# Optimization experiments

Measured on AMD Instinct MI355X. Metric: run time of the kernel, lower is better.

## Reference

```python
import jax, jax.numpy as jnp
import numpy as np
import math

FACTOR = 5  # Informer 'factor' hyperparameter


def setup_inputs() -> dict:
    key = jax.random.key(0)
    B, L, H, D = 2, 2048, 16, 128
    k1, k2, k3, k4 = jax.random.split(key, 4)
    queries = jax.random.normal(k1, (B, L, H, D), jnp.float32)
    keys = jax.random.normal(k2, (B, L, H, D), jnp.float32)
    values = jax.random.normal(k3, (B, L, H, D), jnp.float32)
    sample_k = max(1, min(FACTOR * math.ceil(math.log(L)), L))  # u in the paper
    index_sample = jax.random.randint(k4, (L, sample_k), 0, L, dtype=jnp.int32)
    return {"queries": queries, "keys": keys, "values": values,
            "index_sample": index_sample}


def reference(queries, keys, values, index_sample):
    # queries/keys/values: [B, L, H, D] -> [B, H, L, D]
    Q = jnp.swapaxes(queries, 1, 2)
    K = jnp.swapaxes(keys, 1, 2)
    V = jnp.swapaxes(values, 1, 2)
    B, H, L_Q, D = Q.shape
    L_K = K.shape[2]
    # U_part = factor*ceil(ln L_K), clipped to L_K then to L_Q (n_top in _prob_QK)
    n_top = max(1, min(FACTOR * math.ceil(math.log(L_K)), L_K, L_Q))

    # --- _prob_QK: sampled scores ---
    # K_sample: [B, H, L_Q, sample_k, D] (same materialization as torch K_expand gather)
    K_sample = K[:, :, index_sample, :]
    Q_K_sample = jnp.einsum('bhqd,bhqsd->bhqs', Q, K_sample)
    # sparsity measure M: max - mean(over full L_K, per original torch code)
    M = Q_K_sample.max(axis=-1) - Q_K_sample.sum(axis=-1) / L_K  # [B,H,L_Q]
    _, M_top = jax.lax.top_k(M, n_top)  # [B,H,n_top]

    # gather top queries and compute their full attention rows
    Q_reduce = jnp.take_along_axis(Q, M_top[..., None], axis=2)  # [B,H,u,D]
    scores = jnp.einsum('bhud,bhkd->bhuk', Q_reduce, K)  # [B,H,u,L_K]
    scale = 1.0 / math.sqrt(D)
    scores = scores * scale

    # --- initial context (mask_flag=False): mean of V over keys ---
    context = jnp.broadcast_to(V.mean(axis=2, keepdims=True), (B, H, L_Q, D))

    # --- update context at top-query positions ---
    attn = jax.nn.softmax(scores, axis=-1)
    upd = jnp.einsum('bhuk,bhkd->bhud', attn, V)  # [B,H,u,D]
    bi = jnp.arange(B)[:, None, None]
    hi = jnp.arange(H)[None, :, None]
    context = context.at[bi, hi, M_top].set(upd)

    return jnp.swapaxes(context, 1, 2)  # [B, L_Q, H, D]
```

## Files before the change

kernel.cpp:

```cpp
#include <hip/hip_runtime.h>
#include <math.h>

#define B_    2
#define L_    2048
#define H_    16
#define D_    128
#define S_    40
#define NTOP_ 40
#define NCH_  8
#define CHK_  256
#define VCH_  32
#define CAND_ 512

#define SCALE_ 0.08838834764831843f

typedef _Float16 half2_t __attribute__((ext_vector_type(2)));

__device__ __forceinline__ half2_t as_h2(unsigned int u) {
    union { unsigned int u; half2_t h; } x; x.u = u; return x.h;
}
__device__ __forceinline__ unsigned int h2pack(float a, float b) {
    union { half2_t h; unsigned int u; } x;
    x.h[0] = (_Float16)a; x.h[1] = (_Float16)b; return x.u;
}
#if __has_builtin(__builtin_amdgcn_fdot2)
__device__ __forceinline__ float FDOT2(half2_t a, half2_t b, float c) {
    return __builtin_amdgcn_fdot2(a, b, c, false);
}
#else
__device__ __forceinline__ float FDOT2(half2_t a, half2_t b, float c) {
    return c + (float)a[0] * (float)b[0] + (float)a[1] * (float)b[1];
}
#endif

__device__ __forceinline__ unsigned int encf(float f) {
    unsigned int u = __float_as_uint(f);
    return (u & 0x80000000u) ? ~u : (u | 0x80000000u);
}
__device__ __forceinline__ float decf(unsigned int e) {
    unsigned int u = (e & 0x80000000u) ? (e ^ 0x80000000u) : ~e;
    return __uint_as_float(u);
}

__global__ __launch_bounds__(256) void kA_pack_vpart(const float* __restrict__ K,
                                                     const float* __restrict__ V,
                                                     unsigned int* __restrict__ Kf,
                                                     float* __restrict__ vpart,
                                                     int npack) {
    const int bid = blockIdx.x, t = threadIdx.x;
    if (bid < npack) {
        const int bh = bid >> 3, kc = bid & 7;
        const int h = bh & 15, b = bh >> 4;
        const float4* K4 = (const float4*)K;
        uint2* out2 = (uint2*)Kf;
        for (int j = 0; j < 32; ++j) {
            const int g = j * 256 + t;
            const int row = g >> 5, c = g & 31;
            const float4 v = K4[((size_t)(b * L_ + kc * 256 + row) * H_ + h) * 32 + c];
            out2[(size_t)(bh * L_ + kc * 256 + row) * 32 + c] =
                make_uint2(h2pack(v.x, v.y), h2pack(v.z, v.w));
        }
    } else {
        __shared__ float red[256];
        const int vbid = bid - npack;
        const int bh  = vbid >> 5;
        const int lc  = vbid & (VCH_ - 1);
        const int h   = bh & 15, b = bh >> 4;
        const int d   = t & (D_ - 1);
        const int sub = t >> 7;
        float acc = 0.0f;
        const int l0 = lc * (L_ / VCH_);
        for (int l = l0 + sub; l < l0 + L_ / VCH_; l += 2)
            acc += V[((size_t)(b * L_ + l) * H_ + h) * D_ + d];
        red[t] = acc;
        __syncthreads();
        if (t < D_) vpart[(size_t)vbid * D_ + t] = red[t] + red[t + 128];
    }
}

__global__ __launch_bounds__(256) void k1_sample_f16(const float* __restrict__ Q,
                                                     const uint4* __restrict__ KF,
                                                     const int* __restrict__ idx,
                                                     float* __restrict__ M) {
    const int sb   = blockIdx.x;
    const int xcd  = sb & 7;
    const int li   = sb >> 3;
    const int bh   = (xcd << 2) + (li >> 9);
    const int rb   = li & 511;
    const int t    = threadIdx.x;
    const int wave = t >> 6, lane = t & 63;
    const int q    = rb * 4 + wave;
    const int h    = bh & 15, b = bh >> 4;
    const int g    = lane >> 3, sub = lane & 7;

    const float4* Q4 = (const float4*)Q;
    const size_t rowQ = ((size_t)(b * L_ + q) * H_ + h) * 32;
    const int* ip = idx + q * S_;
    int kidx[5];
    #pragma unroll
    for (int s = 0; s < 5; ++s) kidx[s] = ip[s * 8 + g];

    const float4 qa0 = Q4[rowQ + 2 * sub];
    const float4 qa1 = Q4[rowQ + 2 * sub + 1];
    const float4 qb0 = Q4[rowQ + 16 + 2 * sub];
    const float4 qb1 = Q4[rowQ + 16 + 2 * sub + 1];

    uint4 kv[5][2];
    #pragma unroll
    for (int s = 0; s < 5; ++s) {
        const uint4* kr = KF + ((size_t)bh * L_ + kidx[s]) * 16;
        kv[s][0] = kr[sub];
        kv[s][1] = kr[8 + sub];
    }
    __builtin_amdgcn_sched_barrier(0);

    half2_t qh[8];
    qh[0][0] = (_Float16)qa0.x; qh[0][1] = (_Float16)qa0.y;
    qh[1][0] = (_Float16)qa0.z; qh[1][1] = (_Float16)qa0.w;
    qh[2][0] = (_Float16)qa1.x; qh[2][1] = (_Float16)qa1.y;
    qh[3][0] = (_Float16)qa1.z; qh[3][1] = (_Float16)qa1.w;
    qh[4][0] = (_Float16)qb0.x; qh[4][1] = (_Float16)qb0.y;
    qh[5][0] = (_Float16)qb0.z; qh[5][1] = (_Float16)qb0.w;
    qh[6][0] = (_Float16)qb1.x; qh[6][1] = (_Float16)qb1.y;
    qh[7][0] = (_Float16)qb1.z; qh[7][1] = (_Float16)qb1.w;

    float smax = -INFINITY, ssum = 0.0f;
    #pragma unroll
    for (int s = 0; s < 5; ++s) {
        float p = 0.f;
        p = FDOT2(qh[0], as_h2(kv[s][0].x), p);
        p = FDOT2(qh[1], as_h2(kv[s][0].y), p);
        p = FDOT2(qh[2], as_h2(kv[s][0].z), p);
        p = FDOT2(qh[3], as_h2(kv[s][0].w), p);
        p = FDOT2(qh[4], as_h2(kv[s][1].x), p);
        p = FDOT2(qh[5], as_h2(kv[s][1].y), p);
        p = FDOT2(qh[6], as_h2(kv[s][1].z), p);
        p = FDOT2(qh[7], as_h2(kv[s][1].w), p);
        p += __shfl_xor(p, 1);
        p += __shfl_xor(p, 2);
        p += __shfl_xor(p, 4);
        smax = fmaxf(smax, p);
        ssum += p;
    }
    #pragma unroll
    for (int o = 8; o < 64; o <<= 1) {
        smax = fmaxf(smax, __shfl_xor(smax, o));
        ssum += __shfl_xor(ssum, o);
    }
    if (lane == 0) M[(size_t)bh * L_ + q] = smax - ssum * (1.0f / L_);
}

__global__ __launch_bounds__(256) void k1_sample_f32(const float* __restrict__ Q,
                                                     const float* __restrict__ K,
                                                     const int* __restrict__ idx,
                                                     float* __restrict__ M) {
    const int sb   = blockIdx.x;
    const int xcd  = sb & 7;
    const int li   = sb >> 3;
    const int bh   = (xcd << 2) + (li >> 9);
    const int rb   = li & 511;
    const int t    = threadIdx.x;
    const int wave = t >> 6, lane = t & 63;
    const int q    = rb * 4 + wave;
    const int h    = bh & 15, b = bh >> 4;
    const int g    = lane >> 3, sub = lane & 7;

    const float4* Q4 = (const float4*)Q;
    const float4* K4 = (const float4*)K;
    const size_t rowQ = ((size_t)(b * L_ + q) * H_ + h) * 32;
    const size_t kbase = ((size_t)b * L_ * H_ + h) * 32 + sub;
    const int* ip = idx + q * S_;
    int kidx[5];
    #pragma unroll
    for (int s = 0; s < 5; ++s) kidx[s] = ip[s * 8 + g];
    const float4 qv0 = Q4[rowQ + 0 + sub];
    const float4 qv1 = Q4[rowQ + 8 + sub];
    const float4 qv2 = Q4[rowQ + 16 + sub];
    const float4 qv3 = Q4[rowQ + 24 + sub];
    float4 kv[5][4];
    #pragma unroll
    for (int s = 0; s < 5; ++s) {
        const float4* kb = K4 + kbase + (size_t)kidx[s] * (H_ * 32);
        kv[s][0] = kb[0]; kv[s][1] = kb[8]; kv[s][2] = kb[16]; kv[s][3] = kb[24];
    }
    __builtin_amdgcn_sched_barrier(0);
    float smax = -INFINITY, ssum = 0.0f;
    #pragma unroll
    for (int s = 0; s < 5; ++s) {
        float p = qv0.x * kv[s][0].x + qv0.y * kv[s][0].y + qv0.z * kv[s][0].z + qv0.w * kv[s][0].w
                + qv1.x * kv[s][1].x + qv1.y * kv[s][1].y + qv1.z * kv[s][1].z + qv1.w * kv[s][1].w
                + qv2.x * kv[s][2].x + qv2.y * kv[s][2].y + qv2.z * kv[s][2].z + qv2.w * kv[s][2].w
                + qv3.x * kv[s][3].x + qv3.y * kv[s][3].y + qv3.z * kv[s][3].z + qv3.w * kv[s][3].w;
        p += __shfl_xor(p, 1);
        p += __shfl_xor(p, 2);
        p += __shfl_xor(p, 4);
        smax = fmaxf(smax, p);
        ssum += p;
    }
    #pragma unroll
    for (int o = 8; o < 64; o <<= 1) {
        smax = fmaxf(smax, __shfl_xor(smax, o));
        ssum += __shfl_xor(ssum, o);
    }
    if (lane == 0) M[(size_t)bh * L_ + q] = smax - ssum * (1.0f / L_);
}

__global__ __launch_bounds__(1024) void k2_rank_refine(const float* __restrict__ Mws,
                                                       const float* __restrict__ Q,
                                                       const float* __restrict__ K,
                                                       const int* __restrict__ idx,
                                                       const float* __restrict__ vpart,
                                                       float* __restrict__ vmean,
                                                       int* __restrict__ topk,
                                                       float delta) {
    const int bid = blockIdx.x, t = threadIdx.x;
    if (bid == 32) {
        for (int e = t; e < 32 * D_; e += 1024) {
            const int bh = e >> 7, d = e & 127;
            float s = 0.f;
            #pragma unroll
            for (int c = 0; c < VCH_; ++c)
                s += vpart[(size_t)(bh * VCH_ + c) * D_ + d];
            vmean[e] = s * (1.0f / L_);
        }
        return;
    }
    __shared__ unsigned int ue[L_];
    __shared__ int hist[256], sscan[256];
    __shared__ int sh_chosen, sh_need, sh_nc;
    __shared__ int clist[CAND_];
    __shared__ float cMx[CAND_];
    __shared__ unsigned int cmaxe[CAND_];
    __shared__ float csum[CAND_];
    const int bh = bid, h = bh & 15, b = bh >> 4;
    const float* Mrow = Mws + (size_t)bh * L_;
    for (int i = t; i < L_; i += 1024) ue[i] = encf(Mrow[i]);
    if (t == 0) sh_nc = 0;
    __syncthreads();

    unsigned int prefix = 0; int need = NTOP_;
    for (int l = 3; l >= 0; --l) {
        if (t < 256) hist[t] = 0;
        __syncthreads();
        for (int i = t; i < L_; i += 1024) {
            const unsigned int u = ue[i];
            const bool match = (l == 3) || ((u >> (8 * (l + 1))) == prefix);
            if (match) atomicAdd(&hist[(u >> (8 * l)) & 255], 1);
        }
        __syncthreads();
        if (t < 256) sscan[t] = hist[t];
        __syncthreads();
        for (int off = 1; off < 256; off <<= 1) {
            int v = 0;
            if (t < 256 && t + off < 256) v = sscan[t + off];
            __syncthreads();
            if (t < 256) sscan[t] += v;
            __syncthreads();
        }
        if (t < 256) {
            const int above = sscan[t] - hist[t];
            if (above < need && need <= above + hist[t]) { sh_chosen = t; sh_need = need - above; }
        }
        __syncthreads();
        prefix = (prefix << 8) | (unsigned int)sh_chosen;
        need = sh_need;
        __syncthreads();
    }
    const unsigned int ethr = encf(decf(prefix) - delta);
    for (int i = t; i < L_; i += 1024) {
        if (ue[i] >= ethr) {
            const int p = atomicAdd(&sh_nc, 1);
            if (p < CAND_) clist[p] = i;
        }
    }
    __syncthreads();
    const int nc = min(sh_nc, CAND_);
    for (int i = t; i < CAND_; i += 1024) { cmaxe[i] = 0x007FFFFFu; csum[i] = 0.f; }
    __syncthreads();

    const float4* Q4 = (const float4*)Q;
    const float4* K4 = (const float4*)K;
    const int grp = t >> 3, sub = t & 7;
    for (int task = grp; task < nc * S_; task += 128) {
        const int ci = task / S_;
        const int s  = task - ci * S_;
        const int qq = clist[ci];
        const int ki = idx[qq * S_ + s];
        const float4* Kr = K4 + ((size_t)(b * L_ + ki) * H_ + h) * 32;
        const float4* Qr = Q4 + ((size_t)(b * L_ + qq) * H_ + h) * 32;
        float p = 0.f;
        #pragma unroll
        for (int qt2 = 0; qt2 < 4; ++qt2) {
            const float4 kv = Kr[qt2 * 8 + sub];
            const float4 qv = Qr[qt2 * 8 + sub];
            p += qv.x * kv.x + qv.y * kv.y + qv.z * kv.z + qv.w * kv.w;
        }
        p += __shfl_xor(p, 1);
        p += __shfl_xor(p, 2);
        p += __shfl_xor(p, 4);
        if (sub == 0) {
            atomicMax(&cmaxe[ci], encf(p));
            atomicAdd(&csum[ci], p);
        }
    }
    __syncthreads();
    if (t < nc) cMx[t] = decf(cmaxe[t]) - csum[t] * (1.0f / L_);
    __syncthreads();
    if (t < nc) {
        const float mi = cMx[t]; const int qi = clist[t];
        int rk = 0;
        for (int j = 0; j < nc; ++j) {
            const float mj = cMx[j];
            rk += (mj > mi) || (mj == mi && clist[j] < qi);
        }
        if (rk < NTOP_) topk[bh * NTOP_ + rk] = qi;
    }
}

__global__ __launch_bounds__(512) void k3_scorepv_fill(const float* __restrict__ Q,
                                                       const float* __restrict__ K,
                                                       const float* __restrict__ V,
                                                       const int* __restrict__ topk,
                                                       const float* __restrict__ vmean,
                                                       float* __restrict__ pmax,
                                                       float* __restrict__ psum,
                                                       float* __restrict__ pout,
                                                       float* __restrict__ out) {
    __shared__ float Qs[20 * 132];
    __shared__ float S[20 * 260];
    __shared__ float2 Ppv[20][64];
    __shared__ float mrow[20];
    __shared__ int   tq[20];
    const int bid0 = blockIdx.x;
    const int t   = threadIdx.x;

    if (bid0 >= 512) {
        const int fb = bid0 - 512;
        const float4* vm4 = (const float4*)vmean;
        float4* out4 = (float4*)out;
        const size_t base = (size_t)fb * 4096;
        #pragma unroll
        for (int k = 0; k < 8; ++k) {
            const size_t i = base + k * 512 + t;
            const int d4 = (int)(i & 31);
            const int h  = (int)((i >> 5) & 15);
            const int b  = (int)(i >> 20);
            out4[i] = vm4[((b << 4) + h) * 32 + d4];
        }
        return;
    }

    const int xcd = bid0 & 7;
    const int loc = bid0 >> 3;
    const int bh  = (xcd << 2) + (loc >> 4);
    const int sub16 = loc & 15;
    const int kc  = sub16 >> 1;
    const int uh  = sub16 & 1;
    const int h   = bh & 15, b = bh >> 4;
    const int w   = t >> 6, lane = t & 63;

    if (t < 20) tq[t] = topk[bh * NTOP_ + uh * 20 + t];
    __syncthreads();

    {
        const float4* Q4 = (const float4*)Q;
        #pragma unroll
        for (int it = 0; it < 2; ++it) {
            const int i = it * 512 + t;
            if (i < 640) {
                const int u = i >> 5, dc = i & 31;
                *(float4*)&Qs[u * 132 + dc * 4] =
                    Q4[((size_t)(b * L_ + tq[u]) * H_ + h) * 32 + dc];
            }
        }
    }
    __syncthreads();

    {
        const int kq2 = t >> 2, ug = t & 3;
        float acc[2][5];
        #pragma unroll
        for (int j = 0; j < 2; ++j)
            #pragma unroll
            for (int uu = 0; uu < 5; ++uu) acc[j][uu] = 0.f;
        const float4* Kb = (const float4*)K +
            ((size_t)(b * L_ + kc * CHK_ + kq2 * 2) * H_ + h) * 32;
        for (int dc = 0; dc < 32; ++dc) {
            float4 qv[5];
            #pragma unroll
            for (int uu = 0; uu < 5; ++uu)
                qv[uu] = *(const float4*)&Qs[(ug * 5 + uu) * 132 + dc * 4];
            #pragma unroll
            for (int j = 0; j < 2; ++j) {
                const float4 kv = Kb[(size_t)j * (H_ * 32) + dc];
                #pragma unroll
                for (int uu = 0; uu < 5; ++uu)
                    acc[j][uu] += qv[uu].x * kv.x + qv[uu].y * kv.y
                                + qv[uu].z * kv.z + qv[uu].w * kv.w;
            }
        }
        #pragma unroll
        for (int j = 0; j < 2; ++j)
            #pragma unroll
            for (int uu = 0; uu < 5; ++uu)
                S[(ug * 5 + uu) * 260 + kq2 * 2 + j] = acc[j][uu] * SCALE_;
    }
    __syncthreads();

    {
        #pragma unroll
        for (int jj = 0; jj < 3; ++jj) {
            const int u = w + 8 * jj;
            if (u < 20) {
                const float* Sr = S + u * 260;
                float v = fmaxf(fmaxf(Sr[lane], Sr[lane + 64]),
                                fmaxf(Sr[lane + 128], Sr[lane + 192]));
                #pragma unroll
                for (int o = 1; o < 64; o <<= 1) v = fmaxf(v, __shfl_xor(v, o, 64));
                if (lane == 0) mrow[u] = v;
            }
        }
    }
    __syncthreads();

    for (int e = t; e < 20 * 256; e += 512) {
        const int u = e >> 8, k = e & 255;
        S[u * 260 + k] = __expf(S[u * 260 + k] - mrow[u]);
    }
    __syncthreads();

    {
        #pragma unroll
        for (int jj = 0; jj < 3; ++jj) {
            const int u = w + 8 * jj;
            if (u < 20) {
                const float* Sr = S + u * 260;
                float v = Sr[lane] + Sr[lane + 64] + Sr[lane + 128] + Sr[lane + 192];
                #pragma unroll
                for (int o = 1; o < 64; o <<= 1) v += __shfl_xor(v, o, 64);
                if (lane == 0) {
                    psum[(bh * NCH_ + kc) * NTOP_ + uh * 20 + u] = v;
                    pmax[(bh * NCH_ + kc) * NTOP_ + uh * 20 + u] = mrow[u];
                }
            }
        }
    }

    {
        const int kr2 = w & 1, ug2 = w >> 1;
        const int d2 = lane;
        float accA[5], accB[5];
        #pragma unroll
        for (int uu = 0; uu < 5; ++uu) { accA[uu] = 0.f; accB[uu] = 0.f; }
        const float2* Vb = (const float2*)(V +
            ((size_t)(b * L_ + kc * CHK_ + kr2 * 128) * H_ + h) * D_) + d2;
        for (int kq = 0; kq < 32; ++kq) {
            const float2 v0 = Vb[(size_t)(kq * 4 + 0) * (H_ * D_ / 2)];
            const float2 v1 = Vb[(size_t)(kq * 4 + 1) * (H_ * D_ / 2)];
            const float2 v2 = Vb[(size_t)(kq * 4 + 2) * (H_ * D_ / 2)];
            const float2 v3 = Vb[(size_t)(kq * 4 + 3) * (H_ * D_ / 2)];
            #pragma unroll
            for (int uu = 0; uu < 5; ++uu) {
                const float4 p = *(const float4*)&S[(ug2 * 5 + uu) * 260 + kr2 * 128 + kq * 4];
                accA[uu] += p.x * v0.x + p.y * v1.x + p.z * v2.x + p.w * v3.x;
                accB[uu] += p.x * v0.y + p.y * v1.y + p.z * v2.y + p.w * v3.y;
            }
        }
        if (kr2 == 1) {
            #pragma unroll
            for (int uu = 0; uu < 5; ++uu)
                Ppv[ug2 * 5 + uu][d2] = make_float2(accA[uu], accB[uu]);
        }
        __syncthreads();
        if (kr2 == 0) {
            #pragma unroll
            for (int uu = 0; uu < 5; ++uu) {
                const float2 o = Ppv[ug2 * 5 + uu][d2];
                float* pb = pout + (((size_t)(bh * NCH_ + kc)) * NTOP_ + uh * 20 + ug2 * 5 + uu) * D_ + d2 * 2;
                *(float2*)pb = make_float2(accA[uu] + o.x, accB[uu] + o.y);
            }
        }
    }
}

__global__ __launch_bounds__(128) void k_comb(const float* __restrict__ pmax,
                                              const float* __restrict__ psum,
                                              const float* __restrict__ pout,
                                              const int* __restrict__ topk,
                                              float* __restrict__ out) {
    const int bid = blockIdx.x;
    const int bh  = bid / NTOP_;
    const int u   = bid - bh * NTOP_;
    const int h   = bh & 15, b = bh >> 4;
    const int t   = threadIdx.x;

    float pm[NCH_];
    float M = -INFINITY;
    #pragma unroll
    for (int c = 0; c < NCH_; ++c) {
        pm[c] = pmax[(bh * NCH_ + c) * NTOP_ + u];
        M = fmaxf(M, pm[c]);
    }
    float ssum = 0.0f, o = 0.0f;
    #pragma unroll
    for (int c = 0; c < NCH_; ++c) {
        const float w = __expf(pm[c] - M);
        ssum += psum[(bh * NCH_ + c) * NTOP_ + u] * w;
        o += pout[((size_t)(bh * NCH_ + c) * NTOP_ + u) * D_ + t] * w;
    }
    const int qi = topk[bh * NTOP_ + u];
    out[((size_t)(b * L_ + qi) * H_ + h) * D_ + t] = o / ssum;
}

extern "C" void kernel_launch(void* const* d_in, const int* in_sizes, int n_in,
                              void* d_out, int out_size, void* d_ws, size_t ws_size,
                              hipStream_t stream) {
    const float* Q  = (const float*)d_in[0];
    const float* K  = (const float*)d_in[1];
    const float* V  = (const float*)d_in[2];
    const int* idx  = (const int*)d_in[3];
    float* out      = (float*)d_out;

    char* ws = (char*)d_ws;
    size_t off = 0;
    float* Mws   = (float*)(ws + off); off += (size_t)65536 * 4;
    float* vpart = (float*)(ws + off); off += (size_t)1024 * 128 * 4;
    float* vmean = (float*)(ws + off); off += (size_t)4096 * 4;
    int*   topk  = (int*)(ws + off);   off += 1280 * 4;
    float* pmax  = (float*)(ws + off); off += (size_t)256 * 40 * 4;
    float* psum  = (float*)(ws + off); off += (size_t)256 * 40 * 4;
    float* pout  = (float*)(ws + off); off += (size_t)256 * 40 * 128 * 4;
    unsigned int* Kf = (unsigned int*)(ws + off);
    const size_t kf_bytes = (size_t)32 * L_ * D_ * 2;
    const bool use_f16 = (ws_size >= off + kf_bytes);

    if (use_f16) {
        hipLaunchKernelGGL(kA_pack_vpart, dim3(256 + 1024), dim3(256), 0, stream,
                           K, V, Kf, vpart, 256);
        hipLaunchKernelGGL(k1_sample_f16, dim3(16384), dim3(256), 0, stream,
                           Q, (const uint4*)Kf, idx, Mws);
    } else {
        hipLaunchKernelGGL(kA_pack_vpart, dim3(1024), dim3(256), 0, stream,
                           K, V, Kf, vpart, 0);
        hipLaunchKernelGGL(k1_sample_f32, dim3(16384), dim3(256), 0, stream,
                           Q, K, idx, Mws);
    }
    hipLaunchKernelGGL(k2_rank_refine, dim3(33), dim3(1024), 0, stream,
                       Mws, Q, K, idx, vpart, vmean, topk, use_f16 ? 0.5f : 0.01f);
    hipLaunchKernelGGL(k3_scorepv_fill, dim3(1024), dim3(512), 0, stream,
                       Q, K, V, topk, vmean, pmax, psum, pout, out);
    hipLaunchKernelGGL(k_comb, dim3(1280), dim3(128), 0, stream,
                       pmax, psum, pout, topk, out);
}
```

Before: 127.9 us.

## Fuse V-mean into pack, move mean fill into sampling, fuse combine via last-block atomic

V mean is now computed directly by 32 blocks that each reduce a full head, which drops the partial buffer and the extra reduction block in the rank kernel. The broadcast fill of the mean context into the output moves into the sampling kernel as extra blocks, using nontemporal stores. The separate combine kernel is removed: the last score/PV block per head, found with an atomic counter plus threadfence, merges the chunk partials itself. This saves one launch and overlaps the fill with sampling, at the cost of a serial tail in the last block and much less parallelism in the V-mean reduction.

After: 505.3 us. +295.0%, slower.

```diff
diff --git a/kernel.cpp b/kernel.cpp
--- a/kernel.cpp
+++ b/kernel.cpp
@@ -9,12 +9,12 @@
 #define NTOP_ 40
 #define NCH_  8
 #define CHK_  256
-#define VCH_  32
 #define CAND_ 512
 
 #define SCALE_ 0.08838834764831843f
 
 typedef _Float16 half2_t __attribute__((ext_vector_type(2)));
+typedef float nf4 __attribute__((ext_vector_type(4)));
 
 __device__ __forceinline__ half2_t as_h2(unsigned int u) {
     union { unsigned int u; half2_t h; } x; x.u = u; return x.h;
@@ -42,10 +42,11 @@
     return __uint_as_float(u);
 }
 
-__global__ __launch_bounds__(256) void kA_pack_vpart(const float* __restrict__ K,
+__global__ __launch_bounds__(256) void kA_pack_vmean(const float* __restrict__ K,
                                                      const float* __restrict__ V,
                                                      unsigned int* __restrict__ Kf,
-                                                     float* __restrict__ vpart,
+                                                     float* __restrict__ vmean,
+                                                     int* __restrict__ done,
                                                      int npack) {
     const int bid = blockIdx.x, t = threadIdx.x;
     if (bid < npack) {
@@ -62,32 +63,49 @@
         }
     } else {
         __shared__ float red[256];
-        const int vbid = bid - npack;
-        const int bh  = vbid >> 5;
-        const int lc  = vbid & (VCH_ - 1);
-        const int h   = bh & 15, b = bh >> 4;
-        const int d   = t & (D_ - 1);
+        const int vb = bid - npack;
+        if (vb == 0 && t < 32) done[t] = 0;
+        const int h = vb & 15, b = vb >> 4;
+        const int d = t & (D_ - 1);
         const int sub = t >> 7;
         float acc = 0.0f;
-        const int l0 = lc * (L_ / VCH_);
-        for (int l = l0 + sub; l < l0 + L_ / VCH_; l += 2)
+        for (int l = sub; l < L_; l += 2)
             acc += V[((size_t)(b * L_ + l) * H_ + h) * D_ + d];
         red[t] = acc;
         __syncthreads();
-        if (t < D_) vpart[(size_t)vbid * D_ + t] = red[t] + red[t + 128];
+        if (t < D_) vmean[vb * D_ + t] = (red[t] + red[t + 128]) * (1.0f / L_);
     }
 }
 
 __global__ __launch_bounds__(256) void k1_sample_f16(const float* __restrict__ Q,
                                                      const uint4* __restrict__ KF,
                                                      const int* __restrict__ idx,
-                                                     float* __restrict__ M) {
-    const int sb   = blockIdx.x;
-    const int xcd  = sb & 7;
-    const int li   = sb >> 3;
+                                                     const float* __restrict__ vmean,
+                                                     float* __restrict__ M,
+                                                     float* __restrict__ out) {
+    const int bid = blockIdx.x;
+    const int t   = threadIdx.x;
+
+    if (bid >= 16384) {
+        const int fb = bid - 16384;
+        const nf4* vm4 = (const nf4*)vmean;
+        nf4* out4 = (nf4*)out;
+        const size_t base = (size_t)fb * 4096;
+        #pragma unroll
+        for (int k = 0; k < 16; ++k) {
+            const size_t i = base + k * 256 + t;
+            const int d4 = (int)(i & 31);
+            const int h  = (int)((i >> 5) & 15);
+            const int b  = (int)(i >> 20);
+            __builtin_nontemporal_store(vm4[((b << 4) + h) * 32 + d4], &out4[i]);
+        }
+        return;
+    }
+
+    const int xcd  = bid & 7;
+    const int li   = bid >> 3;
     const int bh   = (xcd << 2) + (li >> 9);
     const int rb   = li & 511;
-    const int t    = threadIdx.x;
     const int wave = t >> 6, lane = t & 63;
     const int q    = rb * 4 + wave;
     const int h    = bh & 15, b = bh >> 4;
@@ -153,13 +171,30 @@
 __global__ __launch_bounds__(256) void k1_sample_f32(const float* __restrict__ Q,
                                                      const float* __restrict__ K,
                                                      const int* __restrict__ idx,
-                                                     float* __restrict__ M) {
-    const int sb   = blockIdx.x;
-    const int xcd  = sb & 7;
-    const int li   = sb >> 3;
+                                                     const float* __restrict__ vmean,
+                                                     float* __restrict__ M,
+                                                     float* __restrict__ out) {
+    const int bid = blockIdx.x;
+    const int t   = threadIdx.x;
+    if (bid >= 16384) {
+        const int fb = bid - 16384;
+        const nf4* vm4 = (const nf4*)vmean;
+        nf4* out4 = (nf4*)out;
+        const size_t base = (size_t)fb * 4096;
+        #pragma unroll
+        for (int k = 0; k < 16; ++k) {
+            const size_t i = base + k * 256 + t;
+            const int d4 = (int)(i & 31);
+            const int h  = (int)((i >> 5) & 15);
+            const int b  = (int)(i >> 20);
+            __builtin_nontemporal_store(vm4[((b << 4) + h) * 32 + d4], &out4[i]);
+        }
+        return;
+    }
+    const int xcd  = bid & 7;
+    const int li   = bid >> 3;
     const int bh   = (xcd << 2) + (li >> 9);
     const int rb   = li & 511;
-    const int t    = threadIdx.x;
     const int wave = t >> 6, lane = t & 63;
     const int q    = rb * 4 + wave;
     const int h    = bh & 15, b = bh >> 4;
@@ -209,22 +244,8 @@
                                                        const float* __restrict__ Q,
                                                        const float* __restrict__ K,
                                                        const int* __restrict__ idx,
-                                                       const float* __restrict__ vpart,
-                                                       float* __restrict__ vmean,
                                                        int* __restrict__ topk,
                                                        float delta) {
-    const int bid = blockIdx.x, t = threadIdx.x;
-    if (bid == 32) {
-        for (int e = t; e < 32 * D_; e += 1024) {
-            const int bh = e >> 7, d = e & 127;
-            float s = 0.f;
-            #pragma unroll
-            for (int c = 0; c < VCH_; ++c)
-                s += vpart[(size_t)(bh * VCH_ + c) * D_ + d];
-            vmean[e] = s * (1.0f / L_);
-        }
-        return;
-    }
     __shared__ unsigned int ue[L_];
     __shared__ int hist[256], sscan[256];
     __shared__ int sh_chosen, sh_need, sh_nc;
@@ -232,6 +253,7 @@
     __shared__ float cMx[CAND_];
     __shared__ unsigned int cmaxe[CAND_];
     __shared__ float csum[CAND_];
+    const int bid = blockIdx.x, t = threadIdx.x;
     const int bh = bid, h = bh & 15, b = bh >> 4;
     const float* Mrow = Mws + (size_t)bh * L_;
     for (int i = t; i < L_; i += 1024) ue[i] = encf(Mrow[i]);
@@ -317,38 +339,23 @@
     }
 }
 
-__global__ __launch_bounds__(512) void k3_scorepv_fill(const float* __restrict__ Q,
-                                                       const float* __restrict__ K,
-                                                       const float* __restrict__ V,
-                                                       const int* __restrict__ topk,
-                                                       const float* __restrict__ vmean,
-                                                       float* __restrict__ pmax,
-                                                       float* __restrict__ psum,
-                                                       float* __restrict__ pout,
-                                                       float* __restrict__ out) {
+__global__ __launch_bounds__(512) void k3_scorepv(const float* __restrict__ Q,
+                                                  const float* __restrict__ K,
+                                                  const float* __restrict__ V,
+                                                  const int* __restrict__ topk,
+                                                  float* __restrict__ pmax,
+                                                  float* __restrict__ psum,
+                                                  float* __restrict__ pout,
+                                                  int* __restrict__ done,
+                                                  float* __restrict__ out) {
     __shared__ float Qs[20 * 132];
     __shared__ float S[20 * 260];
     __shared__ float2 Ppv[20][64];
     __shared__ float mrow[20];
     __shared__ int   tq[20];
+    __shared__ int   lastflag;
     const int bid0 = blockIdx.x;
     const int t   = threadIdx.x;
-
-    if (bid0 >= 512) {
-        const int fb = bid0 - 512;
-        const float4* vm4 = (const float4*)vmean;
-        float4* out4 = (float4*)out;
-        const size_t base = (size_t)fb * 4096;
-        #pragma unroll
-        for (int k = 0; k < 8; ++k) {
-            const size_t i = base + k * 512 + t;
-            const int d4 = (int)(i & 31);
-            const int h  = (int)((i >> 5) & 15);
-            const int b  = (int)(i >> 20);
-            out4[i] = vm4[((b << 4) + h) * 32 + d4];
-        }
-        return;
-    }
 
     const int xcd = bid0 & 7;
     const int loc = bid0 >> 3;
@@ -481,35 +488,36 @@
             }
         }
     }
-}
-
-__global__ __launch_bounds__(128) void k_comb(const float* __restrict__ pmax,
-                                              const float* __restrict__ psum,
-                                              const float* __restrict__ pout,
-                                              const int* __restrict__ topk,
-                                              float* __restrict__ out) {
-    const int bid = blockIdx.x;
-    const int bh  = bid / NTOP_;
-    const int u   = bid - bh * NTOP_;
-    const int h   = bh & 15, b = bh >> 4;
-    const int t   = threadIdx.x;
-
-    float pm[NCH_];
-    float M = -INFINITY;
-    #pragma unroll
-    for (int c = 0; c < NCH_; ++c) {
-        pm[c] = pmax[(bh * NCH_ + c) * NTOP_ + u];
-        M = fmaxf(M, pm[c]);
-    }
-    float ssum = 0.0f, o = 0.0f;
-    #pragma unroll
-    for (int c = 0; c < NCH_; ++c) {
-        const float w = __expf(pm[c] - M);
-        ssum += psum[(bh * NCH_ + c) * NTOP_ + u] * w;
-        o += pout[((size_t)(bh * NCH_ + c) * NTOP_ + u) * D_ + t] * w;
-    }
-    const int qi = topk[bh * NTOP_ + u];
-    out[((size_t)(b * L_ + qi) * H_ + h) * D_ + t] = o / ssum;
+
+    __syncthreads();
+    __threadfence();
+    if (t == 0) {
+        const int old = atomicAdd(&done[bh], 1);
+        lastflag = (old == 15);
+    }
+    __syncthreads();
+    if (lastflag) {
+        __threadfence();
+        for (int e = t; e < NTOP_ * D_; e += 512) {
+            const int u = e >> 7, d = e & (D_ - 1);
+            float pm[NCH_];
+            float Mx = -INFINITY;
+            #pragma unroll
+            for (int c = 0; c < NCH_; ++c) {
+                pm[c] = pmax[(bh * NCH_ + c) * NTOP_ + u];
+                Mx = fmaxf(Mx, pm[c]);
+            }
+            float ssum = 0.0f, o = 0.0f;
+            #pragma unroll
+            for (int c = 0; c < NCH_; ++c) {
+                const float wgt = __expf(pm[c] - Mx);
+                ssum += psum[(bh * NCH_ + c) * NTOP_ + u] * wgt;
+                o += pout[((size_t)(bh * NCH_ + c) * NTOP_ + u) * D_ + d] * wgt;
+            }
+            const int qi = topk[bh * NTOP_ + u];
+            out[((size_t)(b * L_ + qi) * H_ + h) * D_ + d] = o / ssum;
+        }
+    }
 }
 
 extern "C" void kernel_launch(void* const* d_in, const int* in_sizes, int n_in,
@@ -524,9 +532,9 @@
     char* ws = (char*)d_ws;
     size_t off = 0;
     float* Mws   = (float*)(ws + off); off += (size_t)65536 * 4;
-    float* vpart = (float*)(ws + off); off += (size_t)1024 * 128 * 4;
     float* vmean = (float*)(ws + off); off += (size_t)4096 * 4;
     int*   topk  = (int*)(ws + off);   off += 1280 * 4;
+    int*   done  = (int*)(ws + off);   off += 32 * 4;
     float* pmax  = (float*)(ws + off); off += (size_t)256 * 40 * 4;
     float* psum  = (float*)(ws + off); off += (size_t)256 * 40 * 4;
     float* pout  = (float*)(ws + off); off += (size_t)256 * 40 * 128 * 4;
@@ -535,20 +543,18 @@
     const bool use_f16 = (ws_size >= off + kf_bytes);
 
     if (use_f16) {
-        hipLaunchKernelGGL(kA_pack_vpart, dim3(256 + 1024), dim3(256), 0, stream,
-                           K, V, Kf, vpart, 256);
-        hipLaunchKernelGGL(k1_sample_f16, dim3(16384), dim3(256), 0, stream,
-                           Q, (const uint4*)Kf, idx, Mws);
+        hipLaunchKernelGGL(kA_pack_vmean, dim3(256 + 32), dim3(256), 0, stream,
+                           K, V, Kf, vmean, done, 256);
+        hipLaunchKernelGGL(k1_sample_f16, dim3(16384 + 512), dim3(256), 0, stream,
+                           Q, (const uint4*)Kf, idx, vmean, Mws, out);
     } else {
-        hipLaunchKernelGGL(kA_pack_vpart, dim3(1024), dim3(256), 0, stream,
-                           K, V, Kf, vpart, 0);
-        hipLaunchKernelGGL(k1_sample_f32, dim3(16384), dim3(256), 0, stream,
-                           Q, K, idx, Mws);
-    }
-    hipLaunchKernelGGL(k2_rank_refine, dim3(33), dim3(1024), 0, stream,
-                       Mws, Q, K, idx, vpart, vmean, topk, use_f16 ? 0.5f : 0.01f);
-    hipLaunchKernelGGL(k3_scorepv_fill, dim3(1024), dim3(512), 0, stream,
-                       Q, K, V, topk, vmean, pmax, psum, pout, out);
-    hipLaunchKernelGGL(k_comb, dim3(1280), dim3(128), 0, stream,
-                       pmax, psum, pout, topk, out);
-}
+        hipLaunchKernelGGL(kA_pack_vmean, dim3(32), dim3(256), 0, stream,
+                           K, V, Kf, vmean, done, 0);
+        hipLaunchKernelGGL(k1_sample_f32, dim3(16384 + 512), dim3(256), 0, stream,
+                           Q, K, idx, vmean, Mws, out);
+    }
+    hipLaunchKernelGGL(k2_rank_refine, dim3(32), dim3(1024), 0, stream,
+                       Mws, Q, K, idx, topk, use_f16 ? 0.5f : 0.01f);
+    hipLaunchKernelGGL(k3_scorepv, dim3(512), dim3(512), 0, stream,
+                       Q, K, V, topk, pmax, psum, pout, done, out);
+}
```
